# Kernel optimization log

Measured on AMD Instinct MI355X. Metric: run time of the kernel, lower is better.

The kernel has to match this reference:

```python
import jax, jax.numpy as jnp
import numpy as np

ROPE_THETA = 10000.0


def apply_rope(q, k, cos, sin):
    # q,k: [B,H,S,D]; cos,sin: [S,D/2] -> broadcast [1,1,S,D/2]
    def rot(t):
        t2 = t.reshape(*t.shape[:-1], -1, 2)  # [B,H,S,D/2,2]
        te, to = t2[..., 0], t2[..., 1]
        c = cos[None, None, :, :]
        s = sin[None, None, :, :]
        re = te * c - to * s
        im = te * s + to * c
        return jnp.stack([re, im], axis=-1).reshape(t.shape)
    return rot(q), rot(k)


def setup_inputs() -> dict:
    key = jax.random.key(0)
    ks = jax.random.split(key, 4)
    B, S, D, H = 2, 2048, 1024, 16
    hd = D // H
    x = jax.random.normal(ks[0], (B, S, D), dtype=jnp.float32)
    # causal boolean mask (True = keep)
    mask = jnp.tril(jnp.ones((S, S), dtype=bool))[None, None]
    # rotary tables
    inv_freq = 1.0 / (ROPE_THETA ** (jnp.arange(0, hd, 2, dtype=jnp.float32) / hd))  # [hd/2]
    t = jnp.arange(S, dtype=jnp.float32)
    ang = t[:, None] * inv_freq[None, :]  # [S, hd/2]
    freqs_cos = jnp.cos(ang)
    freqs_sin = jnp.sin(ang)
    W_qkv = jax.random.normal(ks[1], (D, 3 * D), dtype=jnp.float32) * 0.02
    b_qkv = jnp.zeros((3 * D,), dtype=jnp.float32)
    W_o = jax.random.normal(ks[2], (D, D), dtype=jnp.float32) * 0.02
    b_o = jnp.zeros((D,), dtype=jnp.float32)
    return {"x": x, "mask": mask, "freqs_cos": freqs_cos, "freqs_sin": freqs_sin,
            "W_qkv": W_qkv, "b_qkv": b_qkv, "W_o": W_o, "b_o": b_o}


def reference(x, mask, freqs_cos, freqs_sin, W_qkv, b_qkv, W_o, b_o):
    B, S, D = x.shape
    H = 16
    hd = D // H
    scale = hd ** -0.5
    qkv = x @ W_qkv + b_qkv  # [B,S,3D]
    q, k, v = jnp.split(qkv, 3, axis=-1)
    q = q.reshape(B, S, H, hd).transpose(0, 2, 1, 3)  # [B,H,S,hd]
    k = k.reshape(B, S, H, hd).transpose(0, 2, 1, 3)
    v = v.reshape(B, S, H, hd).transpose(0, 2, 1, 3)
    q, k = apply_rope(q, k, freqs_cos, freqs_sin)
    scores = jnp.einsum('bhqd,bhkd->bhqk', q, k) * scale
    scores = jnp.where(mask, scores, jnp.finfo(scores.dtype).min)
    attn = jax.nn.softmax(scores, axis=-1)
    out = jnp.einsum('bhqk,bhkd->bhqd', attn, v)
    out = out.transpose(0, 2, 1, 3).reshape(B, S, D)
    return out @ W_o + b_o
```

## Files before the change

### kernel.cpp

```cpp
#include <hip/hip_runtime.h>
#include <hip/hip_bf16.h>
#include <stdint.h>

typedef unsigned short u16;
typedef __attribute__((ext_vector_type(8))) __bf16 bf16x8;
typedef __attribute__((ext_vector_type(4))) float f32x4;
typedef __attribute__((ext_vector_type(16))) float f32x16;
typedef __attribute__((ext_vector_type(8))) u16 u16x8;

__device__ __forceinline__ u16 f2bf(float f) {
  union { float f; unsigned int u; } v; v.f = f;
  unsigned int r = v.u + 0x7fffu + ((v.u >> 16) & 1u);
  return (u16)(r >> 16);
}
__device__ __forceinline__ unsigned pack2(float lo, float hi) {
  return (unsigned)f2bf(lo) | ((unsigned)f2bf(hi) << 16);
}

__device__ __forceinline__ f32x4 mfma16(bf16x8 a, bf16x8 b, f32x4 c) {
  return __builtin_amdgcn_mfma_f32_16x16x32_bf16(a, b, c, 0, 0, 0);
}
__device__ __forceinline__ f32x16 mfma32(bf16x8 a, bf16x8 b, f32x16 c) {
  return __builtin_amdgcn_mfma_f32_32x32x16_bf16(a, b, c, 0, 0, 0);
}

__device__ __forceinline__ void gload16(const void* g, void* l) {
  __builtin_amdgcn_global_load_lds((const __attribute__((address_space(1))) void*)g,
                                   (__attribute__((address_space(3))) void*)l,
                                   16, 0, 0);
}

__global__ void cast_bf16_kernel(const float* __restrict__ in, u16* __restrict__ out, int n) {
  int i = (blockIdx.x * 256 + threadIdx.x) * 8;
  if (i >= n) return;
  const float4* p = (const float4*)(in + i);
  float4 a = p[0], b = p[1];
  u16x8 o;
  o[0] = f2bf(a.x); o[1] = f2bf(a.y); o[2] = f2bf(a.z); o[3] = f2bf(a.w);
  o[4] = f2bf(b.x); o[5] = f2bf(b.y); o[6] = f2bf(b.z); o[7] = f2bf(b.w);
  *(u16x8*)(out + i) = o;
}

__global__ void transpose_cast_k(const float* __restrict__ in, u16* __restrict__ out,
                                 int R, int Ccols) {
  __shared__ float tile[64][65];
  const int c0 = (int)blockIdx.x << 6, r0 = (int)blockIdx.y << 6;
  const int tx = threadIdx.x & 63, ty = threadIdx.x >> 6;
#pragma unroll
  for (int i = ty; i < 64; i += 4)
    tile[i][tx] = in[(size_t)(r0 + i) * Ccols + c0 + tx];
  __syncthreads();
#pragma unroll
  for (int i = ty; i < 64; i += 4)
    out[(size_t)(c0 + i) * R + r0 + tx] = f2bf(tile[tx][i]);
}

__global__ __launch_bounds__(256, 3)
void gemm_qkv(const u16* __restrict__ A, const u16* __restrict__ Bt,
              const float* __restrict__ bias,
              const float* __restrict__ fc, const float* __restrict__ fs,
              u16* __restrict__ qr, u16* __restrict__ kr, u16* __restrict__ vtc) {
  const int K = 1024;
  __shared__ __align__(16) u16 smem[128 * 136];
  u16* const As = smem;
  u16* const Bs = smem + 8192;
  const int m0 = (int)(blockIdx.x / 24) << 7;
  const int n0 = (int)(blockIdx.x % 24) << 7;
  const int tid = threadIdx.x;
  const int l = tid & 63, lg = l >> 4, ll = l & 15;
  const int w = tid >> 6;
  const int wr = (w >> 1) << 6, wc = (w & 1) << 6;
  const int srow = tid >> 2, scol = (tid & 3) << 3;
  const u16* ga = A + (size_t)(m0 + srow) * K + scol;
  const u16* gb = Bt + (size_t)(n0 + srow) * K + scol;
  const size_t K64 = (size_t)64 * K;
  u16* const la00 = &As[srow * 32 + scol];
  u16* const la01 = &As[4096 + srow * 32 + scol];
  u16* const la10 = &As[(srow + 64) * 32 + scol];
  u16* const la11 = &As[4096 + (srow + 64) * 32 + scol];
  u16* const lb00 = &Bs[srow * 32 + scol];
  u16* const lb01 = &Bs[4096 + srow * 32 + scol];
  u16* const lb10 = &Bs[(srow + 64) * 32 + scol];
  u16* const lb11 = &Bs[4096 + (srow + 64) * 32 + scol];
  f32x4 acc[4][4] = {};
  for (int kt = 0; kt < K; kt += 64) {
    gload16(ga + kt, la00);       gload16(ga + kt + 32, la01);
    gload16(ga + kt + K64, la10); gload16(ga + kt + K64 + 32, la11);
    gload16(gb + kt, lb00);       gload16(gb + kt + 32, lb01);
    gload16(gb + kt + K64, lb10); gload16(gb + kt + K64 + 32, lb11);
    __syncthreads();
#pragma unroll
    for (int h = 0; h < 2; ++h) {
      bf16x8 a[4], b[4];
#pragma unroll
      for (int i = 0; i < 4; ++i) {
        a[i] = *(const bf16x8*)&As[h * 4096 + (wr + i * 16 + ll) * 32 + lg * 8];
        b[i] = *(const bf16x8*)&Bs[h * 4096 + (wc + i * 16 + ll) * 32 + lg * 8];
      }
#pragma unroll
      for (int mi = 0; mi < 4; ++mi)
#pragma unroll
        for (int ni = 0; ni < 4; ++ni)
          acc[mi][ni] = mfma16(a[mi], b[ni], acc[mi][ni]);
    }
    __syncthreads();
  }
  const int sec = n0 >> 10;
  const int h0 = (n0 & 1023) >> 6;
#pragma unroll
  for (int ni = 0; ni < 4; ++ni) {
    const int cc = wc + ni * 16 + ll;
    const int n = n0 + cc;
    const int d = n & 63;
    const float bi_ = bias[n];
    const int i2 = d >> 1;
    const bool odd = d & 1;
#pragma unroll
    for (int mi = 0; mi < 4; ++mi) {
#pragma unroll
      for (int r = 0; r < 4; ++r) {
        const int rr = wr + mi * 16 + lg * 4 + r;
        const int s = (m0 + rr) & 2047;
        float v = acc[mi][ni][r] + bi_;
        if (sec < 2) {
          const float c = fc[s * 32 + i2], sn = fs[s * 32 + i2];
          const float p = __shfl_xor(v, 1);
          v = odd ? (p * sn + v * c) : (v * c - p * sn);
          if (sec == 0) v *= 0.125f;
          smem[rr * 136 + cc] = f2bf(v);
        } else {
          smem[cc * 136 + rr] = f2bf(v);
        }
      }
    }
  }
  __syncthreads();
  if (sec < 2) {
    u16* const dst = (sec == 0) ? qr : kr;
#pragma unroll
    for (int it = 0; it < 8; ++it) {
      const int c = it * 256 + tid;
      const int j = c & 7, hh = (c >> 3) & 1, rr = c >> 4;
      const int row = m0 + rr;
      const int bb = row >> 11, ss = row & 2047;
      const uint4 val = *(const uint4*)&smem[rr * 136 + hh * 64 + j * 8];
      *(uint4*)&dst[((size_t)(((bb << 4) + h0 + hh) << 11) + ss) * 64 + j * 8] = val;
    }
  } else {
    const int b16 = (m0 >> 11) << 4;
    const int chbase = (m0 & 2047) >> 6;
#pragma unroll
    for (int it = 0; it < 8; ++it) {
      const int c = it * 256 + tid;
      const int j2 = c & 7;
      const int rr2 = c >> 3;
      const int d = rr2 & 63, hh = (rr2 >> 6) & 1, chk = rr2 >> 7;
      const uint4 val = *(const uint4*)&smem[(hh * 64 + d) * 136 + chk * 64 + j2 * 8];
      *(uint4*)&vtc[(((size_t)(b16 + h0 + hh)) * 32 + chbase + chk) * 4096 + d * 64 + j2 * 8] = val;
    }
  }
}

__global__ __launch_bounds__(256, 2)
void gemm_bt(const u16* __restrict__ A, const u16* __restrict__ Bt,
             const float* __restrict__ bias, float* __restrict__ C,
             int M, int N, int K) {
  __shared__ __align__(16) u16 As[2 * 128 * 32];
  __shared__ __align__(16) u16 Bs[2 * 128 * 32];
  const int nb = N >> 7;
  const int m0 = (int)(blockIdx.x / nb) << 7;
  const int n0 = (int)(blockIdx.x % nb) << 7;
  const int tid = threadIdx.x;
  const int l = tid & 63, lg = l >> 4, ll = l & 15;
  const int w = tid >> 6;
  const int wr = (w >> 1) << 6, wc = (w & 1) << 6;
  const int srow = tid >> 2, scol = (tid & 3) << 3;
  const u16* ga = A + (size_t)(m0 + srow) * K + scol;
  const u16* gb = Bt + (size_t)(n0 + srow) * K + scol;
  const size_t K64 = (size_t)64 * K;
  u16* const la00 = &As[srow * 32 + scol];
  u16* const la01 = &As[4096 + srow * 32 + scol];
  u16* const la10 = &As[(srow + 64) * 32 + scol];
  u16* const la11 = &As[4096 + (srow + 64) * 32 + scol];
  u16* const lb00 = &Bs[srow * 32 + scol];
  u16* const lb01 = &Bs[4096 + srow * 32 + scol];
  u16* const lb10 = &Bs[(srow + 64) * 32 + scol];
  u16* const lb11 = &Bs[4096 + (srow + 64) * 32 + scol];
  f32x4 acc[4][4] = {};
  for (int kt = 0; kt < K; kt += 64) {
    gload16(ga + kt, la00);       gload16(ga + kt + 32, la01);
    gload16(ga + kt + K64, la10); gload16(ga + kt + K64 + 32, la11);
    gload16(gb + kt, lb00);       gload16(gb + kt + 32, lb01);
    gload16(gb + kt + K64, lb10); gload16(gb + kt + K64 + 32, lb11);
    __syncthreads();
#pragma unroll
    for (int h = 0; h < 2; ++h) {
      bf16x8 a[4], b[4];
#pragma unroll
      for (int i = 0; i < 4; ++i) {
        a[i] = *(const bf16x8*)&As[h * 4096 + (wr + i * 16 + ll) * 32 + lg * 8];
        b[i] = *(const bf16x8*)&Bs[h * 4096 + (wc + i * 16 + ll) * 32 + lg * 8];
      }
#pragma unroll
      for (int mi = 0; mi < 4; ++mi)
#pragma unroll
        for (int ni = 0; ni < 4; ++ni)
          acc[mi][ni] = mfma16(a[mi], b[ni], acc[mi][ni]);
    }
    __syncthreads();
  }
#pragma unroll
  for (int mi = 0; mi < 4; ++mi) {
#pragma unroll
    for (int r = 0; r < 4; ++r) {
      const int row = m0 + wr + mi * 16 + lg * 4 + r;
      float* crow = C + (size_t)row * N + n0 + wc;
#pragma unroll
      for (int ni = 0; ni < 4; ++ni)
        crow[ni * 16 + ll] = acc[mi][ni][r] + bias[n0 + wc + ni * 16 + ll];
    }
  }
}

__global__ __launch_bounds__(256, 2)
void attn_k(const u16* __restrict__ qr, const u16* __restrict__ kr,
            const u16* __restrict__ vtc, u16* __restrict__ aout) {
  __shared__ __align__(16) char kvlds[16384];
  const int bi = (int)blockIdx.x;
  const int bh = bi & 31;
  const int qt = (bi < 256) ? (15 - (bi >> 5)) : ((bi - 256) >> 5);
  const int tid = threadIdx.x;
  const int w = tid >> 6, l = tid & 63, hi = l >> 5, ql = l & 31;
  const u16* Q  = qr + (size_t)bh * (2048 * 64);
  const u16* Kp = kr + (size_t)bh * (2048 * 64);
  const int q0w = (qt << 7) + (w << 5);
  const int qg = q0w + ql;
  bf16x8 qf[4];
#pragma unroll
  for (int mi = 0; mi < 4; ++mi)
    qf[mi] = *(const bf16x8*)&Q[(size_t)qg * 64 + mi * 16 + hi * 8];
  const int sr = tid >> 2, sc = (tid & 3) * 32;
  const int wo0 = (sr * 128 + sc) ^ ((sr & 7) << 4);
  const int wo1 = (sr * 128 + sc + 16) ^ ((sr & 7) << 4);
  const char* kga = (const char*)(Kp + (size_t)sr * 64) + sc;
  const char* vga = (const char*)(vtc + (size_t)bh * 32 * 4096) + sr * 128 + sc;
  const int swz = (ql & 7) << 4;
  f32x16 oa = {}, ob = {};
  float mrow = -1e30f, lp = 0.f;
  const int nch = 2 * qt + 2;
  uint4 sk0 = *(const uint4*)(kga), sk1 = *(const uint4*)(kga + 16);
  uint4 sv0 = *(const uint4*)(vga), sv1 = *(const uint4*)(vga + 16);
  for (int ch = 0; ch < nch; ++ch) {
    asm volatile("s_waitcnt vmcnt(0)" ::: "memory");
    asm volatile("s_barrier" ::: "memory");
    *(uint4*)(kvlds + wo0) = sk0;
    *(uint4*)(kvlds + wo1) = sk1;
    *(uint4*)(kvlds + 8192 + wo0) = sv0;
    *(uint4*)(kvlds + 8192 + wo1) = sv1;
    if (ch + 1 < nch) {
      const size_t kof = (size_t)(ch + 1) * 8192;
      sk0 = *(const uint4*)(kga + kof); sk1 = *(const uint4*)(kga + kof + 16);
      sv0 = *(const uint4*)(vga + kof); sv1 = *(const uint4*)(vga + kof + 16);
    }
    asm volatile("s_waitcnt lgkmcnt(0)" ::: "memory");
    asm volatile("s_barrier" ::: "memory");
    const int kb = ch << 6;
    if (kb > q0w + 31) continue;
    f32x16 s0 = {}, s1 = {};
#pragma unroll
    for (int mi = 0; mi < 4; ++mi) {
      const int cb = mi * 32 + hi * 16;
      const bf16x8 k0 = *(const bf16x8*)(kvlds + ((ql * 128 + cb) ^ swz));
      const bf16x8 k1 = *(const bf16x8*)(kvlds + (((32 + ql) * 128 + cb) ^ swz));
      s0 = mfma32(k0, qf[mi], s0);
      s1 = mfma32(k1, qf[mi], s1);
    }
    if (kb + 63 > q0w) {
#pragma unroll
      for (int r = 0; r < 16; ++r) {
        const int kvo = (r & 3) + 8 * (r >> 2) + 4 * hi;
        if (kb + kvo > qg) s0[r] = -1e30f;
        if (kb + 32 + kvo > qg) s1[r] = -1e30f;
      }
    }
    float mx = s0[0];
#pragma unroll
    for (int r = 1; r < 16; ++r) mx = fmaxf(mx, s0[r]);
#pragma unroll
    for (int r = 0; r < 16; ++r) mx = fmaxf(mx, s1[r]);
    mx = fmaxf(mx, __shfl_xor(mx, 32));
    if (!__all(mx <= mrow + 8.f)) {
      const float mn = fmaxf(mrow, mx);
      const float esc = __expf(mrow - mn);
      mrow = mn;
      lp *= esc;
#pragma unroll
      for (int r = 0; r < 16; ++r) { oa[r] *= esc; ob[r] *= esc; }
    }
    float p0[16], p1[16];
#pragma unroll
    for (int r = 0; r < 16; ++r) {
      p0[r] = __expf(s0[r] - mrow);
      p1[r] = __expf(s1[r] - mrow);
      lp += p0[r] + p1[r];
    }
    bf16x8 pb[4];
#pragma unroll
    for (int s = 0; s < 2; ++s) {
      const float* ps = s ? p1 : p0;
#pragma unroll
      for (int j = 0; j < 2; ++j) {
        const unsigned X0 = pack2(ps[j * 8 + 0], ps[j * 8 + 1]);
        const unsigned X1 = pack2(ps[j * 8 + 2], ps[j * 8 + 3]);
        const unsigned Y0 = pack2(ps[j * 8 + 4], ps[j * 8 + 5]);
        const unsigned Y1 = pack2(ps[j * 8 + 6], ps[j * 8 + 7]);
        const unsigned sX0 = (unsigned)__shfl_xor((int)X0, 32);
        const unsigned sX1 = (unsigned)__shfl_xor((int)X1, 32);
        const unsigned sY0 = (unsigned)__shfl_xor((int)Y0, 32);
        const unsigned sY1 = (unsigned)__shfl_xor((int)Y1, 32);
        union { unsigned u[4]; bf16x8 v; } t;
        t.u[0] = hi ? sY0 : X0;
        t.u[1] = hi ? sY1 : X1;
        t.u[2] = hi ? Y0 : sX0;
        t.u[3] = hi ? Y1 : sX1;
        pb[s * 2 + j] = t.v;
      }
    }
#pragma unroll
    for (int jj = 0; jj < 4; ++jj) {
      const int cb = jj * 32 + hi * 16;
      const bf16x8 va = *(const bf16x8*)(kvlds + 8192 + ((ql * 128 + cb) ^ swz));
      const bf16x8 vb = *(const bf16x8*)(kvlds + 8192 + (((32 + ql) * 128 + cb) ^ swz));
      oa = mfma32(va, pb[jj], oa);
      ob = mfma32(vb, pb[jj], ob);
    }
  }
  lp += __shfl_xor(lp, 32);
  const float inv = 1.0f / lp;
  const int hcol = (bh & 15) << 6;
  const int tok = ((bh >> 4) << 11) + qg;
  unsigned* orow = (unsigned*)(aout + (size_t)tok * 1024 + hcol);
#pragma unroll
  for (int r = 0; r < 16; r += 2) {
    const int d0 = (r & 3) + 8 * (r >> 2) + 4 * hi;
    orow[d0 >> 1]        = pack2(oa[r] * inv, oa[r + 1] * inv);
    orow[(32 + d0) >> 1] = pack2(ob[r] * inv, ob[r + 1] * inv);
  }
}

extern "C" void kernel_launch(void* const* d_in, const int* in_sizes, int n_in,
                              void* d_out, int out_size, void* d_ws, size_t ws_size,
                              hipStream_t stream) {
  const float* x    = (const float*)d_in[0];
  const float* fc   = (const float*)d_in[2];
  const float* fs   = (const float*)d_in[3];
  const float* Wqkv = (const float*)d_in[4];
  const float* bqkv = (const float*)d_in[5];
  const float* Wo   = (const float*)d_in[6];
  const float* bo   = (const float*)d_in[7];
  float* out = (float*)d_out;

  size_t off = 0;
  auto alloc = [&](size_t bytes) {
    void* p = (char*)d_ws + off;
    off += (bytes + 255) & ~(size_t)255;
    return p;
  };
  u16*   xb   = (u16*)  alloc(4096ull * 1024 * 2);
  u16*   wqt  = (u16*)  alloc(3072ull * 1024 * 2);
  u16*   wot  = (u16*)  alloc(1024ull * 1024 * 2);
  u16*   qr_  = (u16*)  alloc(32ull * 2048 * 64 * 2);
  u16*   kr_  = (u16*)  alloc(32ull * 2048 * 64 * 2);
  u16*   vtc_ = (u16*)  alloc(32ull * 32 * 4096 * 2);
  u16*   ao_  = (u16*)  alloc(4096ull * 1024 * 2);

  cast_bf16_kernel<<<2048, 256, 0, stream>>>(x, xb, 4096 * 1024);
  transpose_cast_k<<<dim3(48, 16), 256, 0, stream>>>(Wqkv, wqt, 1024, 3072);
  transpose_cast_k<<<dim3(16, 16), 256, 0, stream>>>(Wo, wot, 1024, 1024);
  gemm_qkv<<<dim3(32 * 24), 256, 0, stream>>>(xb, wqt, bqkv, fc, fs, qr_, kr_, vtc_);
  attn_k<<<dim3(512), 256, 0, stream>>>(qr_, kr_, vtc_, ao_);
  gemm_bt<<<dim3(32 * 8), 256, 0, stream>>>(ao_, wot, bo, out, 4096, 1024, 1024);
}
```

Baseline: 128.9 us.

## Use 256-row query tiles with split-KV for long causal tiles and merge

```diff
diff --git a/kernel.cpp b/kernel.cpp
--- a/kernel.cpp
+++ b/kernel.cpp
@@ -222,42 +222,131 @@
   }
 }
 
-__global__ __launch_bounds__(256, 2)
+#define ATTN_HALF(QF, MROW, LP, OA, OB, QGX, GATE)                              \
+  {                                                                             \
+    f32x16 s0 = {}, s1 = {};                                                    \
+    __builtin_amdgcn_s_setprio(1);                                              \
+    _Pragma("unroll")                                                           \
+    for (int mi = 0; mi < 4; ++mi) {                                            \
+      const int cb = mi * 32 + hi * 16;                                         \
+      const bf16x8 k0 = *(const bf16x8*)(kvlds + ((ql * 128 + cb) ^ swz));      \
+      const bf16x8 k1 = *(const bf16x8*)(kvlds + (((32 + ql) * 128 + cb) ^ swz));\
+      s0 = mfma32(k0, QF[mi], s0);                                              \
+      s1 = mfma32(k1, QF[mi], s1);                                              \
+    }                                                                           \
+    __builtin_amdgcn_s_setprio(0);                                              \
+    if (kb + 63 > (GATE)) {                                                     \
+      _Pragma("unroll")                                                         \
+      for (int r = 0; r < 16; ++r) {                                            \
+        const int kvo = (r & 3) + 8 * (r >> 2) + 4 * hi;                        \
+        if (kb + kvo > (QGX)) s0[r] = -1e30f;                                   \
+        if (kb + 32 + kvo > (QGX)) s1[r] = -1e30f;                              \
+      }                                                                         \
+    }                                                                           \
+    float mx = s0[0];                                                           \
+    _Pragma("unroll")                                                           \
+    for (int r = 1; r < 16; ++r) mx = fmaxf(mx, s0[r]);                         \
+    _Pragma("unroll")                                                           \
+    for (int r = 0; r < 16; ++r) mx = fmaxf(mx, s1[r]);                         \
+    mx = fmaxf(mx, __shfl_xor(mx, 32));                                         \
+    if (!__all(mx <= MROW + 8.f)) {                                             \
+      const float mn = fmaxf(MROW, mx);                                         \
+      const float esc = __expf(MROW - mn);                                      \
+      MROW = mn;                                                                \
+      LP *= esc;                                                                \
+      _Pragma("unroll")                                                         \
+      for (int r = 0; r < 16; ++r) { OA[r] *= esc; OB[r] *= esc; }              \
+    }                                                                           \
+    float p0[16], p1[16];                                                       \
+    _Pragma("unroll")                                                           \
+    for (int r = 0; r < 16; ++r) {                                              \
+      p0[r] = __expf(s0[r] - MROW);                                             \
+      p1[r] = __expf(s1[r] - MROW);                                             \
+      LP += p0[r] + p1[r];                                                      \
+    }                                                                           \
+    bf16x8 pb[4];                                                               \
+    _Pragma("unroll")                                                           \
+    for (int s = 0; s < 2; ++s) {                                               \
+      const float* ps = s ? p1 : p0;                                            \
+      _Pragma("unroll")                                                         \
+      for (int j = 0; j < 2; ++j) {                                             \
+        const unsigned X0 = pack2(ps[j * 8 + 0], ps[j * 8 + 1]);                \
+        const unsigned X1 = pack2(ps[j * 8 + 2], ps[j * 8 + 3]);                \
+        const unsigned Y0 = pack2(ps[j * 8 + 4], ps[j * 8 + 5]);                \
+        const unsigned Y1 = pack2(ps[j * 8 + 6], ps[j * 8 + 7]);                \
+        const unsigned sX0 = (unsigned)__shfl_xor((int)X0, 32);                 \
+        const unsigned sX1 = (unsigned)__shfl_xor((int)X1, 32);                 \
+        const unsigned sY0 = (unsigned)__shfl_xor((int)Y0, 32);                 \
+        const unsigned sY1 = (unsigned)__shfl_xor((int)Y1, 32);                 \
+        union { unsigned u[4]; bf16x8 v; } t;                                   \
+        t.u[0] = hi ? sY0 : X0;                                                 \
+        t.u[1] = hi ? sY1 : X1;                                                 \
+        t.u[2] = hi ? Y0 : sX0;                                                 \
+        t.u[3] = hi ? Y1 : sX1;                                                 \
+        pb[s * 2 + j] = t.v;                                                    \
+      }                                                                         \
+    }                                                                           \
+    __builtin_amdgcn_s_setprio(1);                                              \
+    _Pragma("unroll")                                                           \
+    for (int jj = 0; jj < 4; ++jj) {                                            \
+      const int cb = jj * 32 + hi * 16;                                         \
+      const bf16x8 va = *(const bf16x8*)(kvlds + 8192 + ((ql * 128 + cb) ^ swz));\
+      const bf16x8 vb = *(const bf16x8*)(kvlds + 8192 + (((32 + ql) * 128 + cb) ^ swz));\
+      OA = mfma32(va, pb[jj], OA);                                              \
+      OB = mfma32(vb, pb[jj], OB);                                              \
+    }                                                                           \
+    __builtin_amdgcn_s_setprio(0);                                              \
+  }
+
+__global__ __launch_bounds__(256, 1)
 void attn_k(const u16* __restrict__ qr, const u16* __restrict__ kr,
-            const u16* __restrict__ vtc, u16* __restrict__ aout) {
+            const u16* __restrict__ vtc, u16* __restrict__ aout,
+            float* __restrict__ pO, float* __restrict__ pML) {
   __shared__ __align__(16) char kvlds[16384];
+  const signed char TT[13] = {7,7,6,6,5,5,2,4,4,3,3,1,0};
+  const signed char HH[13] = {0,1,0,1,0,1,0,0,1,0,1,0,0};
+  const signed char SP[13] = {1,1,1,1,1,1,0,1,1,1,1,0,0};
   const int bi = (int)blockIdx.x;
   const int bh = bi & 31;
-  const int qt = (bi < 256) ? (15 - (bi >> 5)) : ((bi - 256) >> 5);
+  const int sidx = bi >> 5;
+  const int t = TT[sidx], half = HH[sidx];
+  const bool split = SP[sidx];
+  const int hlen = 2 * (t + 1);
+  const int ch0 = split ? (half ? hlen : 0) : 0;
+  const int ch1 = split ? (half ? 2 * hlen : hlen) : (4 * (t + 1));
   const int tid = threadIdx.x;
   const int w = tid >> 6, l = tid & 63, hi = l >> 5, ql = l & 31;
   const u16* Q  = qr + (size_t)bh * (2048 * 64);
   const u16* Kp = kr + (size_t)bh * (2048 * 64);
-  const int q0w = (qt << 7) + (w << 5);
-  const int qg = q0w + ql;
-  bf16x8 qf[4];
-#pragma unroll
-  for (int mi = 0; mi < 4; ++mi)
-    qf[mi] = *(const bf16x8*)&Q[(size_t)qg * 64 + mi * 16 + hi * 8];
+  const int q0w = (t << 8) + (w << 6);
+  const int qgA = q0w + ql;
+  const int qgB = q0w + 32 + ql;
+  bf16x8 qfA[4], qfB[4];
+#pragma unroll
+  for (int mi = 0; mi < 4; ++mi) {
+    qfA[mi] = *(const bf16x8*)&Q[(size_t)qgA * 64 + mi * 16 + hi * 8];
+    qfB[mi] = *(const bf16x8*)&Q[(size_t)qgB * 64 + mi * 16 + hi * 8];
+  }
   const int sr = tid >> 2, sc = (tid & 3) * 32;
   const int wo0 = (sr * 128 + sc) ^ ((sr & 7) << 4);
   const int wo1 = (sr * 128 + sc + 16) ^ ((sr & 7) << 4);
   const char* kga = (const char*)(Kp + (size_t)sr * 64) + sc;
   const char* vga = (const char*)(vtc + (size_t)bh * 32 * 4096) + sr * 128 + sc;
   const int swz = (ql & 7) << 4;
-  f32x16 oa = {}, ob = {};
-  float mrow = -1e30f, lp = 0.f;
-  const int nch = 2 * qt + 2;
-  uint4 sk0 = *(const uint4*)(kga), sk1 = *(const uint4*)(kga + 16);
-  uint4 sv0 = *(const uint4*)(vga), sv1 = *(const uint4*)(vga + 16);
-  for (int ch = 0; ch < nch; ++ch) {
+  f32x16 oaA = {}, obA = {}, oaB = {}, obB = {};
+  float mrowA = -1e30f, lpA = 0.f, mrowB = -1e30f, lpB = 0.f;
+  uint4 sk0 = *(const uint4*)(kga + (size_t)ch0 * 8192);
+  uint4 sk1 = *(const uint4*)(kga + (size_t)ch0 * 8192 + 16);
+  uint4 sv0 = *(const uint4*)(vga + (size_t)ch0 * 8192);
+  uint4 sv1 = *(const uint4*)(vga + (size_t)ch0 * 8192 + 16);
+  for (int ch = ch0; ch < ch1; ++ch) {
     asm volatile("s_waitcnt vmcnt(0)" ::: "memory");
     asm volatile("s_barrier" ::: "memory");
     *(uint4*)(kvlds + wo0) = sk0;
     *(uint4*)(kvlds + wo1) = sk1;
     *(uint4*)(kvlds + 8192 + wo0) = sv0;
     *(uint4*)(kvlds + 8192 + wo1) = sv1;
-    if (ch + 1 < nch) {
+    if (ch + 1 < ch1) {
       const size_t kof = (size_t)(ch + 1) * 8192;
       sk0 = *(const uint4*)(kga + kof); sk1 = *(const uint4*)(kga + kof + 16);
       sv0 = *(const uint4*)(vga + kof); sv1 = *(const uint4*)(vga + kof + 16);
@@ -265,87 +354,66 @@
     asm volatile("s_waitcnt lgkmcnt(0)" ::: "memory");
     asm volatile("s_barrier" ::: "memory");
     const int kb = ch << 6;
-    if (kb > q0w + 31) continue;
-    f32x16 s0 = {}, s1 = {};
-#pragma unroll
-    for (int mi = 0; mi < 4; ++mi) {
-      const int cb = mi * 32 + hi * 16;
-      const bf16x8 k0 = *(const bf16x8*)(kvlds + ((ql * 128 + cb) ^ swz));
-      const bf16x8 k1 = *(const bf16x8*)(kvlds + (((32 + ql) * 128 + cb) ^ swz));
-      s0 = mfma32(k0, qf[mi], s0);
-      s1 = mfma32(k1, qf[mi], s1);
-    }
-    if (kb + 63 > q0w) {
-#pragma unroll
-      for (int r = 0; r < 16; ++r) {
-        const int kvo = (r & 3) + 8 * (r >> 2) + 4 * hi;
-        if (kb + kvo > qg) s0[r] = -1e30f;
-        if (kb + 32 + kvo > qg) s1[r] = -1e30f;
-      }
-    }
-    float mx = s0[0];
-#pragma unroll
-    for (int r = 1; r < 16; ++r) mx = fmaxf(mx, s0[r]);
-#pragma unroll
-    for (int r = 0; r < 16; ++r) mx = fmaxf(mx, s1[r]);
-    mx = fmaxf(mx, __shfl_xor(mx, 32));
-    if (!__all(mx <= mrow + 8.f)) {
-      const float mn = fmaxf(mrow, mx);
-      const float esc = __expf(mrow - mn);
-      mrow = mn;
-      lp *= esc;
-#pragma unroll
-      for (int r = 0; r < 16; ++r) { oa[r] *= esc; ob[r] *= esc; }
-    }
-    float p0[16], p1[16];
-#pragma unroll
-    for (int r = 0; r < 16; ++r) {
-      p0[r] = __expf(s0[r] - mrow);
-      p1[r] = __expf(s1[r] - mrow);
-      lp += p0[r] + p1[r];
-    }
-    bf16x8 pb[4];
-#pragma unroll
-    for (int s = 0; s < 2; ++s) {
-      const float* ps = s ? p1 : p0;
-#pragma unroll
-      for (int j = 0; j < 2; ++j) {
-        const unsigned X0 = pack2(ps[j * 8 + 0], ps[j * 8 + 1]);
-        const unsigned X1 = pack2(ps[j * 8 + 2], ps[j * 8 + 3]);
-        const unsigned Y0 = pack2(ps[j * 8 + 4], ps[j * 8 + 5]);
-        const unsigned Y1 = pack2(ps[j * 8 + 6], ps[j * 8 + 7]);
-        const unsigned sX0 = (unsigned)__shfl_xor((int)X0, 32);
-        const unsigned sX1 = (unsigned)__shfl_xor((int)X1, 32);
-        const unsigned sY0 = (unsigned)__shfl_xor((int)Y0, 32);
-        const unsigned sY1 = (unsigned)__shfl_xor((int)Y1, 32);
-        union { unsigned u[4]; bf16x8 v; } t;
-        t.u[0] = hi ? sY0 : X0;
-        t.u[1] = hi ? sY1 : X1;
-        t.u[2] = hi ? Y0 : sX0;
-        t.u[3] = hi ? Y1 : sX1;
-        pb[s * 2 + j] = t.v;
-      }
-    }
-#pragma unroll
-    for (int jj = 0; jj < 4; ++jj) {
-      const int cb = jj * 32 + hi * 16;
-      const bf16x8 va = *(const bf16x8*)(kvlds + 8192 + ((ql * 128 + cb) ^ swz));
-      const bf16x8 vb = *(const bf16x8*)(kvlds + 8192 + (((32 + ql) * 128 + cb) ^ swz));
-      oa = mfma32(va, pb[jj], oa);
-      ob = mfma32(vb, pb[jj], ob);
-    }
-  }
-  lp += __shfl_xor(lp, 32);
-  const float inv = 1.0f / lp;
+    if (kb > q0w + 63) continue;
+    if (kb <= q0w + 31)
+      ATTN_HALF(qfA, mrowA, lpA, oaA, obA, qgA, q0w)
+    ATTN_HALF(qfB, mrowB, lpB, oaB, obB, qgB, q0w + 32)
+  }
+  lpA += __shfl_xor(lpA, 32);
+  lpB += __shfl_xor(lpB, 32);
   const int hcol = (bh & 15) << 6;
-  const int tok = ((bh >> 4) << 11) + qg;
-  unsigned* orow = (unsigned*)(aout + (size_t)tok * 1024 + hcol);
-#pragma unroll
-  for (int r = 0; r < 16; r += 2) {
-    const int d0 = (r & 3) + 8 * (r >> 2) + 4 * hi;
-    orow[d0 >> 1]        = pack2(oa[r] * inv, oa[r + 1] * inv);
-    orow[(32 + d0) >> 1] = pack2(ob[r] * inv, ob[r + 1] * inv);
-  }
+  if (!split) {
+    const float invA = 1.0f / lpA, invB = 1.0f / lpB;
+    const int tokA = ((bh >> 4) << 11) + qgA;
+    const int tokB = ((bh >> 4) << 11) + qgB;
+    unsigned* orowA = (unsigned*)(aout + (size_t)tokA * 1024 + hcol);
+    unsigned* orowB = (unsigned*)(aout + (size_t)tokB * 1024 + hcol);
+#pragma unroll
+    for (int r = 0; r < 16; r += 2) {
+      const int d0 = (r & 3) + 8 * (r >> 2) + 4 * hi;
+      orowA[d0 >> 1]        = pack2(oaA[r] * invA, oaA[r + 1] * invA);
+      orowA[(32 + d0) >> 1] = pack2(obA[r] * invA, obA[r + 1] * invA);
+      orowB[d0 >> 1]        = pack2(oaB[r] * invB, oaB[r + 1] * invB);
+      orowB[(32 + d0) >> 1] = pack2(obB[r] * invB, obB[r + 1] * invB);
+    }
+  } else {
+    const int ridxA = bh * 1280 + (qgA - 768);
+    const int ridxB = bh * 1280 + (qgB - 768);
+    float* prowA = pO + ((size_t)ridxA * 2 + half) * 64;
+    float* prowB = pO + ((size_t)ridxB * 2 + half) * 64;
+#pragma unroll
+    for (int r = 0; r < 16; r += 2) {
+      const int d0 = (r & 3) + 8 * (r >> 2) + 4 * hi;
+      *(float2*)&prowA[d0]      = make_float2(oaA[r], oaA[r + 1]);
+      *(float2*)&prowA[32 + d0] = make_float2(obA[r], obA[r + 1]);
+      *(float2*)&prowB[d0]      = make_float2(oaB[r], oaB[r + 1]);
+      *(float2*)&prowB[32 + d0] = make_float2(obB[r], obB[r + 1]);
+    }
+    if (hi == 0) {
+      pML[((size_t)ridxA * 2 + half) * 2 + 0] = mrowA;
+      pML[((size_t)ridxA * 2 + half) * 2 + 1] = lpA;
+      pML[((size_t)ridxB * 2 + half) * 2 + 0] = mrowB;
+      pML[((size_t)ridxB * 2 + half) * 2 + 1] = lpB;
+    }
+  }
+}
+
+__global__ void attn_merge(const float* __restrict__ pO, const float* __restrict__ pML,
+                           u16* __restrict__ aout) {
+  const int idx = (int)blockIdx.x * 256 + threadIdx.x;
+  const int d = idx & 63;
+  const int rr = idx >> 6;
+  const float mA = pML[rr * 4 + 0], lA = pML[rr * 4 + 1];
+  const float mB = pML[rr * 4 + 2], lB = pML[rr * 4 + 3];
+  const float M = fmaxf(mA, mB);
+  const float eA = __expf(mA - M), eB = __expf(mB - M);
+  const float num = pO[((size_t)rr * 2 + 0) * 64 + d] * eA
+                  + pO[((size_t)rr * 2 + 1) * 64 + d] * eB;
+  const float den = lA * eA + lB * eB;
+  const int bh = rr / 1280, row = (rr % 1280) + 768;
+  const int tok = ((bh >> 4) << 11) + row;
+  const int hcol = (bh & 15) << 6;
+  aout[(size_t)tok * 1024 + hcol + d] = f2bf(num / den);
 }
 
 extern "C" void kernel_launch(void* const* d_in, const int* in_sizes, int n_in,
@@ -373,11 +441,14 @@
   u16*   kr_  = (u16*)  alloc(32ull * 2048 * 64 * 2);
   u16*   vtc_ = (u16*)  alloc(32ull * 32 * 4096 * 2);
   u16*   ao_  = (u16*)  alloc(4096ull * 1024 * 2);
+  float* pO_  = (float*)alloc(32ull * 1280 * 2 * 64 * 4);
+  float* pML_ = (float*)alloc(32ull * 1280 * 2 * 2 * 4);
 
   cast_bf16_kernel<<<2048, 256, 0, stream>>>(x, xb, 4096 * 1024);
   transpose_cast_k<<<dim3(48, 16), 256, 0, stream>>>(Wqkv, wqt, 1024, 3072);
   transpose_cast_k<<<dim3(16, 16), 256, 0, stream>>>(Wo, wot, 1024, 1024);
   gemm_qkv<<<dim3(32 * 24), 256, 0, stream>>>(xb, wqt, bqkv, fc, fs, qr_, kr_, vtc_);
-  attn_k<<<dim3(512), 256, 0, stream>>>(qr_, kr_, vtc_, ao_);
+  attn_k<<<dim3(13 * 32), 256, 0, stream>>>(qr_, kr_, vtc_, ao_, pO_, pML_);
+  attn_merge<<<dim3(10240), 256, 0, stream>>>(pO_, pML_, ao_);
   gemm_bt<<<dim3(32 * 8), 256, 0, stream>>>(ao_, wot, bo, out, 4096, 1024, 1024);
 }
```

Result: slower. 160.2 us (+24.2%).
